# Performance work log

Hardware: AMD Instinct MI355X
Metric: run time of the kernel (lower is better)

## Reference

```python
import jax, jax.numpy as jnp
import numpy as np

B, T, I, H = 8192, 658, 7, 1
D1, D2, D3 = 1024, 512, 128


def setup_inputs() -> dict:
    key = jax.random.key(0)
    ks = jax.random.split(key, 14)
    return {
        "x": jax.random.normal(ks[0], (B, T, I), dtype=jnp.float32),
        "h0": jax.random.uniform(ks[1], (1, B, H), dtype=jnp.float32),
        "W_ih": jax.random.normal(ks[2], (H, I), dtype=jnp.float32) * 0.3,
        "W_hh": jax.random.normal(ks[3], (H, H), dtype=jnp.float32) * 0.3,
        "b_ih": jax.random.normal(ks[4], (H,), dtype=jnp.float32) * 0.1,
        "b_hh": jax.random.normal(ks[5], (H,), dtype=jnp.float32) * 0.1,
        "w1": jax.random.normal(ks[6], (D1, T), dtype=jnp.float32) * 0.03,
        "b1": jax.random.normal(ks[7], (D1,), dtype=jnp.float32) * 0.01,
        "w2": jax.random.normal(ks[8], (D2, D1), dtype=jnp.float32) * 0.03,
        "b2": jax.random.normal(ks[9], (D2,), dtype=jnp.float32) * 0.01,
        "w3": jax.random.normal(ks[10], (D3, D2), dtype=jnp.float32) * 0.03,
        "b3": jax.random.normal(ks[11], (D3,), dtype=jnp.float32) * 0.01,
        "w4": jax.random.normal(ks[12], (T, D3), dtype=jnp.float32) * 0.03,
        "b4": jax.random.normal(ks[13], (T,), dtype=jnp.float32) * 0.01,
    }


def _forward(x, h0, W_ih, W_hh, b_ih, b_hh, w1, b1, w2, b2, w3, b3, w4, b4):
    # Precompute input projection for all timesteps: [T, B, H]
    xw = jnp.einsum("bti,hi->tbh", x, W_ih) + b_ih

    def step(h, xw_t):  # h: [B, H]
        h_new = jnp.tanh(xw_t + h @ W_hh.T + b_hh)
        return h_new, h_new

    h_last, hs = jax.lax.scan(step, h0[0], xw)  # hs: [T, B, H]
    out = jnp.transpose(hs, (1, 0, 2)).reshape(-1, T)  # [B, T] (view(-1, seq))

    out = jax.nn.relu(out @ w1.T + b1)
    out = jax.nn.relu(out @ w2.T + b2)
    out = jax.nn.relu(out @ w3.T + b3)
    out = out @ w4.T + b4
    return out, h_last[None]  # hidden: [1, B, H]


def reference(x, h0, W_ih, W_hh, b_ih, b_hh, w1, b1, w2, b2, w3, b3, w4, b4):
    return _forward(x, h0, W_ih, W_hh, b_ih, b_hh, w1, b1, w2, b2, w3, b3, w4, b4)
```

## Files before the change

kernel.cpp:

```cpp
#include <hip/hip_runtime.h>
#include <hip/hip_bf16.h>
#include <stdint.h>
#include <stddef.h>

#define B_  8192
#define T_  658
#define I_  7
#define TP  672
#define D1_ 1024
#define D2_ 512
#define D3_ 128
#define NP4 768

#define NB  64
#define CT  32
#define NCH 21

#define XWBLKS 21504
#define CVBLKS 5376

typedef __bf16 bf16x8 __attribute__((ext_vector_type(8)));
typedef float  floatx4 __attribute__((ext_vector_type(4)));

__device__ __forceinline__ void gload_lds16(const void* g, void* l) {
    __builtin_amdgcn_global_load_lds(
        (const __attribute__((address_space(1))) void*)g,
        (__attribute__((address_space(3))) void*)l, 16, 0, 0);
}

__device__ __forceinline__ unsigned int pack_bf16x2(float a, float b) {
    unsigned int ua = __float_as_uint(a);
    unsigned int ub = __float_as_uint(b);
    ua += 0x7fffu + ((ua >> 16) & 1u);
    ub += 0x7fffu + ((ub >> 16) & 1u);
    return (ua >> 16) | (ub & 0xffff0000u);
}

__device__ __forceinline__ float bf16lo(unsigned int u) { return __uint_as_float(u << 16); }
__device__ __forceinline__ float bf16hi(unsigned int u) { return __uint_as_float(u & 0xffff0000u); }

__global__ void xw_conv_kernel(const float* __restrict__ x,
                               const float* __restrict__ Wih,
                               const float* __restrict__ bih,
                               __bf16* __restrict__ xwb,
                               const float* __restrict__ w1, const float* __restrict__ w2,
                               const float* __restrict__ w3, const float* __restrict__ w4,
                               __bf16* __restrict__ w1b, __bf16* __restrict__ w2b,
                               __bf16* __restrict__ w3b, __bf16* __restrict__ w4b) {
    if (blockIdx.x < XWBLKS) {
        const int i = blockIdx.x * 256 + threadIdx.x;
        const int b = i / TP, t = i - b * TP;
        float s = 0.0f;
        if (t < T_) {
            const float* xp = x + ((size_t)b * T_ + t) * I_;
            s = bih[0];
#pragma unroll
            for (int j = 0; j < I_; ++j) s = fmaf(xp[j], Wih[j], s);
        }
        xwb[i] = (__bf16)s;
        return;
    }
    int i = (blockIdx.x - XWBLKS) * 256 + threadIdx.x;
    if (i < D1_ * TP) {
        int r = i / TP, c = i - r * TP;
        w1b[i] = (__bf16)(c < T_ ? w1[r * T_ + c] : 0.0f);
        return;
    }
    i -= D1_ * TP;
    if (i < D2_ * D1_) { w2b[i] = (__bf16)w2[i]; return; }
    i -= D2_ * D1_;
    if (i < D3_ * D2_) { w3b[i] = (__bf16)w3[i]; return; }
    i -= D3_ * D2_;
    {
        int r = i / D3_, c = i - r * D3_;
        w4b[i] = (__bf16)(r < T_ ? w4[r * D3_ + c] : 0.0f);
    }
}

__global__ __launch_bounds__(64) void scan_kernel(
    const __bf16* __restrict__ xwb, const float* __restrict__ h0,
    const float* __restrict__ Whh, const float* __restrict__ bhh,
    __bf16* __restrict__ A0, float* __restrict__ hlast) {
    __shared__ float        lds_x[CT * (NB + 1)];
    __shared__ unsigned int lds_o[NB * 17];

    const int tid = threadIdx.x;
    const int b0 = blockIdx.x * NB;
    const float whh = Whh[0], bh = bhh[0];
    const float C2L = 2.8853900817779268f;
    const float whhc = whh * C2L;
    const float m2w = -2.0f * whhc;
    float h = h0[b0 + tid];
    float r = (1.0f - h) * 0.5f;

    uint4 pf[4];
    unsigned int res[CT / 2];

#pragma unroll
    for (int l = 0; l < 4; ++l) {
        const int idx = l * NB + tid;
        const int bl = idx >> 2, q = idx & 3;
        pf[l] = *(const uint4*)(xwb + (size_t)(b0 + bl) * TP + q * 8);
    }

    for (int c = 0; c < NCH; ++c) {
        const int t0 = c * CT;
        __syncthreads();
#pragma unroll
        for (int l = 0; l < 4; ++l) {
            const int idx = l * NB + tid;
            const int bl = idx >> 2, q = idx & 3;
            const uint4 v = pf[l];
            lds_x[(q * 8 + 0) * (NB + 1) + bl] = bf16lo(v.x);
            lds_x[(q * 8 + 1) * (NB + 1) + bl] = bf16hi(v.x);
            lds_x[(q * 8 + 2) * (NB + 1) + bl] = bf16lo(v.y);
            lds_x[(q * 8 + 3) * (NB + 1) + bl] = bf16hi(v.y);
            lds_x[(q * 8 + 4) * (NB + 1) + bl] = bf16lo(v.z);
            lds_x[(q * 8 + 5) * (NB + 1) + bl] = bf16hi(v.z);
            lds_x[(q * 8 + 6) * (NB + 1) + bl] = bf16lo(v.w);
            lds_x[(q * 8 + 7) * (NB + 1) + bl] = bf16hi(v.w);
        }
        if (c > 0) {
#pragma unroll
            for (int j = 0; j < 16; ++j) lds_o[tid * 17 + j] = res[j];
        }
        __syncthreads();
        if (c > 0) {
            const int tprev = t0 - CT;
#pragma unroll
            for (int l = 0; l < 4; ++l) {
                const int idx = l * NB + tid;
                const int bl = idx >> 2, q = idx & 3;
                uint4 v;
                v.x = lds_o[bl * 17 + q * 4 + 0];
                v.y = lds_o[bl * 17 + q * 4 + 1];
                v.z = lds_o[bl * 17 + q * 4 + 2];
                v.w = lds_o[bl * 17 + q * 4 + 3];
                *(uint4*)(A0 + (size_t)(b0 + bl) * TP + tprev + q * 8) = v;
            }
        }
        if (c + 1 < NCH) {
            const int tn = t0 + CT;
#pragma unroll
            for (int l = 0; l < 4; ++l) {
                const int idx = l * NB + tid;
                const int bl = idx >> 2, q = idx & 3;
                pf[l] = *(const uint4*)(xwb + (size_t)(b0 + bl) * TP + tn + q * 8);
            }
        }
        if (c < NCH - 1) {
#pragma unroll
            for (int k = 0; k < CT; k += 2) {
                float xv0 = lds_x[k * (NB + 1) + tid];
                float xv1 = lds_x[(k + 1) * (NB + 1) + tid];
                float c0 = fmaf(xv0 + bh, C2L, whhc);
                float c1 = fmaf(xv1 + bh, C2L, whhc);
                r = __builtin_amdgcn_rcpf(__builtin_amdgcn_exp2f(fmaf(m2w, r, c0)) + 1.0f);
                float h0v = fmaf(-2.0f, r, 1.0f);
                r = __builtin_amdgcn_rcpf(__builtin_amdgcn_exp2f(fmaf(m2w, r, c1)) + 1.0f);
                h = fmaf(-2.0f, r, 1.0f);
                res[k >> 1] = pack_bf16x2(h0v, h);
            }
        } else {
            const int nval = T_ - t0;
#pragma unroll
            for (int k = 0; k < CT; k += 2) {
                float r0 = 0.0f, r1 = 0.0f;
                if (k < nval) {
                    float xv0 = lds_x[k * (NB + 1) + tid];
                    r = __builtin_amdgcn_rcpf(
                        __builtin_amdgcn_exp2f(fmaf(m2w, r, fmaf(xv0 + bh, C2L, whhc))) + 1.0f);
                    h = fmaf(-2.0f, r, 1.0f);
                    r0 = h;
                }
                if (k + 1 < nval) {
                    float xv1 = lds_x[(k + 1) * (NB + 1) + tid];
                    r = __builtin_amdgcn_rcpf(
                        __builtin_amdgcn_exp2f(fmaf(m2w, r, fmaf(xv1 + bh, C2L, whhc))) + 1.0f);
                    h = fmaf(-2.0f, r, 1.0f);
                    r1 = h;
                }
                res[k >> 1] = pack_bf16x2(r0, r1);
            }
        }
    }
    __syncthreads();
#pragma unroll
    for (int j = 0; j < 16; ++j) lds_o[tid * 17 + j] = res[j];
    __syncthreads();
    {
        const int tprev = TP - CT;
#pragma unroll
        for (int l = 0; l < 4; ++l) {
            const int idx = l * NB + tid;
            const int bl = idx >> 2, q = idx & 3;
            uint4 v;
            v.x = lds_o[bl * 17 + q * 4 + 0];
            v.y = lds_o[bl * 17 + q * 4 + 1];
            v.z = lds_o[bl * 17 + q * 4 + 2];
            v.w = lds_o[bl * 17 + q * 4 + 3];
            *(uint4*)(A0 + (size_t)(b0 + bl) * TP + tprev + q * 8) = v;
        }
    }
    hlast[b0 + tid] = h;
}

template<int BM, int BN, int MINW>
__global__ __launch_bounds__(256, MINW) void gemm_bt(
    const __bf16* __restrict__ A, const __bf16* __restrict__ W,
    const float* __restrict__ bias, __bf16* __restrict__ outb,
    float* __restrict__ outf, int K, int Npad, int Nreal, int relu) {
    constexpr int MI = BM / 32;
    constexpr int NJ = BN / 32;
    constexpr int nA = BM / 64;
    constexpr int nB = BN / 64;
    __shared__ __align__(16) __bf16 As[BM * 32];
    __shared__ __align__(16) __bf16 Bs[BN * 32];

    const int tid = threadIdx.x;
    int mb, nb;
    {
        const int nbx = gridDim.x;
        const int bid = blockIdx.y * nbx + blockIdx.x;
        if ((nbx & 7) == 0) {
            const int mpx = nbx >> 3;
            const int xcd = bid & 7, j = bid >> 3;
            mb = xcd * mpx + (j % mpx);
            nb = j / mpx;
        } else {
            mb = blockIdx.x; nb = blockIdx.y;
        }
    }
    const int m0 = mb * BM, n0 = nb * BN;
    const int lane = tid & 63, wave = tid >> 6;
    const int wm = (wave & 1) * (BM / 2), wn = (wave >> 1) * (BN / 2);
    const int quad = lane >> 4, l16 = lane & 15;

    const int eoff = tid * 8;
    const int rowS = eoff >> 5;
    const int colS = eoff & 31;
    const __bf16* gaa[nA];
    const __bf16* gbb[nB];
    __bf16* laa[nA];
    __bf16* lbb[nB];
#pragma unroll
    for (int c = 0; c < nA; ++c) {
        gaa[c] = A + (size_t)(m0 + rowS + c * 64) * K + colS;
        laa[c] = As + c * 2048 + (tid & 192) * 8;
    }
#pragma unroll
    for (int c = 0; c < nB; ++c) {
        gbb[c] = W + (size_t)(n0 + rowS + c * 64) * K + colS;
        lbb[c] = Bs + c * 2048 + (tid & 192) * 8;
    }

    floatx4 acc[MI][NJ] = {};

    for (int k0 = 0; k0 < K; k0 += 32) {
#pragma unroll
        for (int c = 0; c < nA; ++c) gload_lds16(gaa[c] + k0, laa[c]);
#pragma unroll
        for (int c = 0; c < nB; ++c) gload_lds16(gbb[c] + k0, lbb[c]);
        __syncthreads();

        bf16x8 af[MI], bg[NJ];
#pragma unroll
        for (int i = 0; i < MI; ++i)
            af[i] = *(const bf16x8*)(As + (wm + i * 16 + l16) * 32 + quad * 8);
#pragma unroll
        for (int j = 0; j < NJ; ++j)
            bg[j] = *(const bf16x8*)(Bs + (wn + j * 16 + l16) * 32 + quad * 8);
#pragma unroll
        for (int i = 0; i < MI; ++i)
#pragma unroll
            for (int j = 0; j < NJ; ++j)
                acc[i][j] = __builtin_amdgcn_mfma_f32_16x16x32_bf16(af[i], bg[j], acc[i][j], 0, 0, 0);
        __syncthreads();
    }

#pragma unroll
    for (int j = 0; j < NJ; ++j) {
        const int n = n0 + wn + j * 16 + l16;
        const float bv = (n < Nreal) ? bias[n] : 0.0f;
#pragma unroll
        for (int i = 0; i < MI; ++i) {
#pragma unroll
            for (int r = 0; r < 4; ++r) {
                const int m = m0 + wm + i * 16 + quad * 4 + r;
                float v = acc[i][j][r] + bv;
                if (relu) v = fmaxf(v, 0.0f);
                if (outb) {
                    outb[(size_t)m * Npad + n] = (__bf16)v;
                } else if (n < Nreal) {
                    outf[(size_t)m * Nreal + n] = v;
                }
            }
        }
    }
}

extern "C" void kernel_launch(void* const* d_in, const int* in_sizes, int n_in,
                              void* d_out, int out_size, void* d_ws, size_t ws_size,
                              hipStream_t stream) {
    const float* x   = (const float*)d_in[0];
    const float* h0  = (const float*)d_in[1];
    const float* Wih = (const float*)d_in[2];
    const float* Whh = (const float*)d_in[3];
    const float* bih = (const float*)d_in[4];
    const float* bhh = (const float*)d_in[5];
    const float* w1  = (const float*)d_in[6];
    const float* b1  = (const float*)d_in[7];
    const float* w2  = (const float*)d_in[8];
    const float* b2  = (const float*)d_in[9];
    const float* w3  = (const float*)d_in[10];
    const float* b3  = (const float*)d_in[11];
    const float* w4  = (const float*)d_in[12];
    const float* b4  = (const float*)d_in[13];
    float* out = (float*)d_out;
    char* ws = (char*)d_ws;

    __bf16* w1b = (__bf16*)(ws + 0);
    __bf16* w2b = (__bf16*)(ws + 1376256);
    __bf16* w3b = (__bf16*)(ws + 2424832);
    __bf16* w4b = (__bf16*)(ws + 2555904);
    __bf16* A0  = (__bf16*)(ws + 2752512);
    __bf16* A1  = (__bf16*)(ws + 13762560);
    __bf16* A2  = (__bf16*)(ws + 30539776);
    __bf16* A3  = (__bf16*)(ws + 38928384);
    __bf16* xwb = (__bf16*)(ws + 13762560);

    xw_conv_kernel<<<XWBLKS + CVBLKS, 256, 0, stream>>>(
        x, Wih, bih, xwb, w1, w2, w3, w4, w1b, w2b, w3b, w4b);
    scan_kernel<<<128, 64, 0, stream>>>(xwb, h0, Whh, bhh, A0, out + (size_t)B_ * T_);

    gemm_bt<128,128,2><<<dim3(64, 8), 256, 0, stream>>>(A0, w1b, b1, A1, nullptr, TP,  D1_, D1_, 1);
    gemm_bt<128,64,4> <<<dim3(64, 8), 256, 0, stream>>>(A1, w2b, b2, A2, nullptr, D1_, D2_, D2_, 1);
    gemm_bt<64,64,4>  <<<dim3(128, 2), 256, 0, stream>>>(A2, w3b, b3, A3, nullptr, D2_, D3_, D3_, 1);
    gemm_bt<64,128,4> <<<dim3(128, 6), 256, 0, stream>>>(A3, w4b, b4, nullptr, out, D3_, NP4, T_, 0);
}
```

Measured before the change: 336.1 us.

## Fuse input projection into scan kernel with warp-specialized producer pipeline

Removes the separate xw precompute pass and its bf16 intermediate buffer. The scan kernel now uses 256-thread blocks of 32 batch rows each. Three wavefronts compute x·W_ih into double-buffered LDS for the next chunk, while one wavefront runs the recurrence and another stores the previous chunk's outputs. This doubles the scan block count to 256 and removes a global round trip of the projection, but only 32 lanes do the serial recurrence per block and there is a barrier per chunk. The weight conversion blocks are folded into the same launch, and the second GEMM's min-waves launch bound changes from 4 to 2.

Result: slower. 354.2 us (+5.4%).

```diff
diff --git a/kernel.cpp b/kernel.cpp
--- a/kernel.cpp
+++ b/kernel.cpp
@@ -12,11 +12,11 @@
 #define D3_ 128
 #define NP4 768
 
-#define NB  64
+#define NB2 32
 #define CT  32
 #define NCH 21
-
-#define XWBLKS 21504
+#define SCANBLKS 256
+
 #define CVBLKS 5376
 
 typedef __bf16 bf16x8 __attribute__((ext_vector_type(8)));
@@ -36,173 +36,131 @@
     return (ua >> 16) | (ub & 0xffff0000u);
 }
 
-__device__ __forceinline__ float bf16lo(unsigned int u) { return __uint_as_float(u << 16); }
-__device__ __forceinline__ float bf16hi(unsigned int u) { return __uint_as_float(u & 0xffff0000u); }
-
-__global__ void xw_conv_kernel(const float* __restrict__ x,
-                               const float* __restrict__ Wih,
-                               const float* __restrict__ bih,
-                               __bf16* __restrict__ xwb,
-                               const float* __restrict__ w1, const float* __restrict__ w2,
-                               const float* __restrict__ w3, const float* __restrict__ w4,
-                               __bf16* __restrict__ w1b, __bf16* __restrict__ w2b,
-                               __bf16* __restrict__ w3b, __bf16* __restrict__ w4b) {
-    if (blockIdx.x < XWBLKS) {
-        const int i = blockIdx.x * 256 + threadIdx.x;
-        const int b = i / TP, t = i - b * TP;
-        float s = 0.0f;
-        if (t < T_) {
-            const float* xp = x + ((size_t)b * T_ + t) * I_;
-            s = bih[0];
-#pragma unroll
-            for (int j = 0; j < I_; ++j) s = fmaf(xp[j], Wih[j], s);
-        }
-        xwb[i] = (__bf16)s;
+__global__ __launch_bounds__(256) void scan_conv_kernel(
+    const float* __restrict__ x, const float* __restrict__ h0,
+    const float* __restrict__ Wih, const float* __restrict__ Whh,
+    const float* __restrict__ bih, const float* __restrict__ bhh,
+    __bf16* __restrict__ A0, float* __restrict__ hlast,
+    const float* __restrict__ w1, const float* __restrict__ w2,
+    const float* __restrict__ w3, const float* __restrict__ w4,
+    __bf16* __restrict__ w1b, __bf16* __restrict__ w2b,
+    __bf16* __restrict__ w3b, __bf16* __restrict__ w4b) {
+    if (blockIdx.x >= SCANBLKS) {
+        int i = (blockIdx.x - SCANBLKS) * 256 + threadIdx.x;
+        if (i < D1_ * TP) {
+            int r = i / TP, c = i - r * TP;
+            w1b[i] = (__bf16)(c < T_ ? w1[r * T_ + c] : 0.0f);
+            return;
+        }
+        i -= D1_ * TP;
+        if (i < D2_ * D1_) { w2b[i] = (__bf16)w2[i]; return; }
+        i -= D2_ * D1_;
+        if (i < D3_ * D2_) { w3b[i] = (__bf16)w3[i]; return; }
+        i -= D3_ * D2_;
+        {
+            int r = i / D3_, c = i - r * D3_;
+            w4b[i] = (__bf16)(r < T_ ? w4[r * D3_ + c] : 0.0f);
+        }
         return;
     }
-    int i = (blockIdx.x - XWBLKS) * 256 + threadIdx.x;
-    if (i < D1_ * TP) {
-        int r = i / TP, c = i - r * TP;
-        w1b[i] = (__bf16)(c < T_ ? w1[r * T_ + c] : 0.0f);
-        return;
-    }
-    i -= D1_ * TP;
-    if (i < D2_ * D1_) { w2b[i] = (__bf16)w2[i]; return; }
-    i -= D2_ * D1_;
-    if (i < D3_ * D2_) { w3b[i] = (__bf16)w3[i]; return; }
-    i -= D3_ * D2_;
-    {
-        int r = i / D3_, c = i - r * D3_;
-        w4b[i] = (__bf16)(r < T_ ? w4[r * D3_ + c] : 0.0f);
-    }
-}
-
-__global__ __launch_bounds__(64) void scan_kernel(
-    const __bf16* __restrict__ xwb, const float* __restrict__ h0,
-    const float* __restrict__ Whh, const float* __restrict__ bhh,
-    __bf16* __restrict__ A0, float* __restrict__ hlast) {
-    __shared__ float        lds_x[CT * (NB + 1)];
-    __shared__ unsigned int lds_o[NB * 17];
+
+    __shared__ float        lds_x[2][CT][NB2 + 1];
+    __shared__ unsigned int lds_o[2][NB2 * 17];
 
     const int tid = threadIdx.x;
-    const int b0 = blockIdx.x * NB;
-    const float whh = Whh[0], bh = bhh[0];
+    const int b0 = blockIdx.x * NB2;
+
+    const float whh = Whh[0], bh = bhh[0], bi = bih[0];
+    float wih[I_];
+#pragma unroll
+    for (int j = 0; j < I_; ++j) wih[j] = Wih[j];
+
     const float C2L = 2.8853900817779268f;
     const float whhc = whh * C2L;
     const float m2w = -2.0f * whhc;
-    float h = h0[b0 + tid];
-    float r = (1.0f - h) * 0.5f;
-
-    uint4 pf[4];
+
+    float h = 0.0f, r = 0.0f;
+    if (tid < NB2) {
+        h = h0[b0 + tid];
+        r = (1.0f - h) * 0.5f;
+    }
     unsigned int res[CT / 2];
 
-#pragma unroll
-    for (int l = 0; l < 4; ++l) {
-        const int idx = l * NB + tid;
-        const int bl = idx >> 2, q = idx & 3;
-        pf[l] = *(const uint4*)(xwb + (size_t)(b0 + bl) * TP + q * 8);
-    }
-
-    for (int c = 0; c < NCH; ++c) {
-        const int t0 = c * CT;
+    for (int it = 0; it < NCH + 2; ++it) {
+        if (it < NCH && tid >= 64) {
+            const int ptid = tid - 64;
+            const int t0 = it * CT;
+#pragma unroll
+            for (int j = 0; j < 6; ++j) {
+                const int cell = ptid + j * 192;
+                if (cell < NB2 * CT) {
+                    const int bl = cell >> 5, tt = cell & 31;
+                    const int t = t0 + tt;
+                    float s = 0.0f;
+                    if (t < T_) {
+                        const float* xp = x + ((size_t)(b0 + bl) * T_ + t) * I_;
+                        s = bi;
+#pragma unroll
+                        for (int i = 0; i < I_; ++i) s = fmaf(xp[i], wih[i], s);
+                    }
+                    lds_x[it & 1][tt][bl] = s;
+                }
+            }
+        }
+        if (tid < NB2 && it >= 1 && it <= NCH) {
+            const int ck = it - 1;
+            const float* lx = &lds_x[ck & 1][0][tid];
+            if (ck < NCH - 1) {
+#pragma unroll
+                for (int k = 0; k < CT; k += 2) {
+                    float xv0 = lx[k * (NB2 + 1)];
+                    float xv1 = lx[(k + 1) * (NB2 + 1)];
+                    float c0 = fmaf(xv0 + bh, C2L, whhc);
+                    float c1 = fmaf(xv1 + bh, C2L, whhc);
+                    r = __builtin_amdgcn_rcpf(__builtin_amdgcn_exp2f(fmaf(m2w, r, c0)) + 1.0f);
+                    float h0v = fmaf(-2.0f, r, 1.0f);
+                    r = __builtin_amdgcn_rcpf(__builtin_amdgcn_exp2f(fmaf(m2w, r, c1)) + 1.0f);
+                    h = fmaf(-2.0f, r, 1.0f);
+                    res[k >> 1] = pack_bf16x2(h0v, h);
+                }
+            } else {
+                const int nval = T_ - ck * CT;
+#pragma unroll
+                for (int k = 0; k < CT; k += 2) {
+                    float r0 = 0.0f, r1 = 0.0f;
+                    if (k < nval) {
+                        float xv0 = lx[k * (NB2 + 1)];
+                        r = __builtin_amdgcn_rcpf(
+                            __builtin_amdgcn_exp2f(fmaf(m2w, r, fmaf(xv0 + bh, C2L, whhc))) + 1.0f);
+                        h = fmaf(-2.0f, r, 1.0f);
+                        r0 = h;
+                    }
+                    if (k + 1 < nval) {
+                        float xv1 = lx[(k + 1) * (NB2 + 1)];
+                        r = __builtin_amdgcn_rcpf(
+                            __builtin_amdgcn_exp2f(fmaf(m2w, r, fmaf(xv1 + bh, C2L, whhc))) + 1.0f);
+                        h = fmaf(-2.0f, r, 1.0f);
+                        r1 = h;
+                    }
+                    res[k >> 1] = pack_bf16x2(r0, r1);
+                }
+            }
+#pragma unroll
+            for (int j = 0; j < 16; ++j) lds_o[ck & 1][tid * 17 + j] = res[j];
+        }
+        if (it >= 2 && tid < 128) {
+            const int ck = it - 2;
+            const int bl = tid >> 2, q = tid & 3;
+            uint4 v;
+            v.x = lds_o[ck & 1][bl * 17 + q * 4 + 0];
+            v.y = lds_o[ck & 1][bl * 17 + q * 4 + 1];
+            v.z = lds_o[ck & 1][bl * 17 + q * 4 + 2];
+            v.w = lds_o[ck & 1][bl * 17 + q * 4 + 3];
+            *(uint4*)(A0 + (size_t)(b0 + bl) * TP + ck * CT + q * 8) = v;
+        }
         __syncthreads();
-#pragma unroll
-        for (int l = 0; l < 4; ++l) {
-            const int idx = l * NB + tid;
-            const int bl = idx >> 2, q = idx & 3;
-            const uint4 v = pf[l];
-            lds_x[(q * 8 + 0) * (NB + 1) + bl] = bf16lo(v.x);
-            lds_x[(q * 8 + 1) * (NB + 1) + bl] = bf16hi(v.x);
-            lds_x[(q * 8 + 2) * (NB + 1) + bl] = bf16lo(v.y);
-            lds_x[(q * 8 + 3) * (NB + 1) + bl] = bf16hi(v.y);
-            lds_x[(q * 8 + 4) * (NB + 1) + bl] = bf16lo(v.z);
-            lds_x[(q * 8 + 5) * (NB + 1) + bl] = bf16hi(v.z);
-            lds_x[(q * 8 + 6) * (NB + 1) + bl] = bf16lo(v.w);
-            lds_x[(q * 8 + 7) * (NB + 1) + bl] = bf16hi(v.w);
-        }
-        if (c > 0) {
-#pragma unroll
-            for (int j = 0; j < 16; ++j) lds_o[tid * 17 + j] = res[j];
-        }
-        __syncthreads();
-        if (c > 0) {
-            const int tprev = t0 - CT;
-#pragma unroll
-            for (int l = 0; l < 4; ++l) {
-                const int idx = l * NB + tid;
-                const int bl = idx >> 2, q = idx & 3;
-                uint4 v;
-                v.x = lds_o[bl * 17 + q * 4 + 0];
-                v.y = lds_o[bl * 17 + q * 4 + 1];
-                v.z = lds_o[bl * 17 + q * 4 + 2];
-                v.w = lds_o[bl * 17 + q * 4 + 3];
-                *(uint4*)(A0 + (size_t)(b0 + bl) * TP + tprev + q * 8) = v;
-            }
-        }
-        if (c + 1 < NCH) {
-            const int tn = t0 + CT;
-#pragma unroll
-            for (int l = 0; l < 4; ++l) {
-                const int idx = l * NB + tid;
-                const int bl = idx >> 2, q = idx & 3;
-                pf[l] = *(const uint4*)(xwb + (size_t)(b0 + bl) * TP + tn + q * 8);
-            }
-        }
-        if (c < NCH - 1) {
-#pragma unroll
-            for (int k = 0; k < CT; k += 2) {
-                float xv0 = lds_x[k * (NB + 1) + tid];
-                float xv1 = lds_x[(k + 1) * (NB + 1) + tid];
-                float c0 = fmaf(xv0 + bh, C2L, whhc);
-                float c1 = fmaf(xv1 + bh, C2L, whhc);
-                r = __builtin_amdgcn_rcpf(__builtin_amdgcn_exp2f(fmaf(m2w, r, c0)) + 1.0f);
-                float h0v = fmaf(-2.0f, r, 1.0f);
-                r = __builtin_amdgcn_rcpf(__builtin_amdgcn_exp2f(fmaf(m2w, r, c1)) + 1.0f);
-                h = fmaf(-2.0f, r, 1.0f);
-                res[k >> 1] = pack_bf16x2(h0v, h);
-            }
-        } else {
-            const int nval = T_ - t0;
-#pragma unroll
-            for (int k = 0; k < CT; k += 2) {
-                float r0 = 0.0f, r1 = 0.0f;
-                if (k < nval) {
-                    float xv0 = lds_x[k * (NB + 1) + tid];
-                    r = __builtin_amdgcn_rcpf(
-                        __builtin_amdgcn_exp2f(fmaf(m2w, r, fmaf(xv0 + bh, C2L, whhc))) + 1.0f);
-                    h = fmaf(-2.0f, r, 1.0f);
-                    r0 = h;
-                }
-                if (k + 1 < nval) {
-                    float xv1 = lds_x[(k + 1) * (NB + 1) + tid];
-                    r = __builtin_amdgcn_rcpf(
-                        __builtin_amdgcn_exp2f(fmaf(m2w, r, fmaf(xv1 + bh, C2L, whhc))) + 1.0f);
-                    h = fmaf(-2.0f, r, 1.0f);
-                    r1 = h;
-                }
-                res[k >> 1] = pack_bf16x2(r0, r1);
-            }
-        }
-    }
-    __syncthreads();
-#pragma unroll
-    for (int j = 0; j < 16; ++j) lds_o[tid * 17 + j] = res[j];
-    __syncthreads();
-    {
-        const int tprev = TP - CT;
-#pragma unroll
-        for (int l = 0; l < 4; ++l) {
-            const int idx = l * NB + tid;
-            const int bl = idx >> 2, q = idx & 3;
-            uint4 v;
-            v.x = lds_o[bl * 17 + q * 4 + 0];
-            v.y = lds_o[bl * 17 + q * 4 + 1];
-            v.z = lds_o[bl * 17 + q * 4 + 2];
-            v.w = lds_o[bl * 17 + q * 4 + 3];
-            *(uint4*)(A0 + (size_t)(b0 + bl) * TP + tprev + q * 8) = v;
-        }
-    }
-    hlast[b0 + tid] = h;
+    }
+    if (tid < NB2) hlast[b0 + tid] = h;
 }
 
 template<int BM, int BN, int MINW>
@@ -327,14 +285,13 @@
     __bf16* A1  = (__bf16*)(ws + 13762560);
     __bf16* A2  = (__bf16*)(ws + 30539776);
     __bf16* A3  = (__bf16*)(ws + 38928384);
-    __bf16* xwb = (__bf16*)(ws + 13762560);
-
-    xw_conv_kernel<<<XWBLKS + CVBLKS, 256, 0, stream>>>(
-        x, Wih, bih, xwb, w1, w2, w3, w4, w1b, w2b, w3b, w4b);
-    scan_kernel<<<128, 64, 0, stream>>>(xwb, h0, Whh, bhh, A0, out + (size_t)B_ * T_);
+
+    scan_conv_kernel<<<SCANBLKS + CVBLKS, 256, 0, stream>>>(
+        x, h0, Wih, Whh, bih, bhh, A0, out + (size_t)B_ * T_,
+        w1, w2, w3, w4, w1b, w2b, w3b, w4b);
 
     gemm_bt<128,128,2><<<dim3(64, 8), 256, 0, stream>>>(A0, w1b, b1, A1, nullptr, TP,  D1_, D1_, 1);
-    gemm_bt<128,64,4> <<<dim3(64, 8), 256, 0, stream>>>(A1, w2b, b2, A2, nullptr, D1_, D2_, D2_, 1);
+    gemm_bt<128,64,2> <<<dim3(64, 8), 256, 0, stream>>>(A1, w2b, b2, A2, nullptr, D1_, D2_, D2_, 1);
     gemm_bt<64,64,4>  <<<dim3(128, 2), 256, 0, stream>>>(A2, w3b, b3, A3, nullptr, D2_, D3_, D3_, 1);
     gemm_bt<64,128,4> <<<dim3(128, 6), 256, 0, stream>>>(A3, w4b, b4, nullptr, out, D3_, NP4, T_, 0);
 }
```
